# Optimization experiments

Hardware: AMD Instinct MI355X
Metric: run time of the kernel (lower is better)

The kernel has to match this reference:

```python
import jax, jax.numpy as jnp
import numpy as np

M, N, B, L = 512, 2048, 4, 20
H_DENSITY = 0.02  # Tanner graph sparsity: row weight ~N*p=40, col weight ~M*p=10


def setup_inputs() -> dict:
    key = jax.random.key(0)
    ks = jax.random.split(key, 10)
    H = jax.random.bernoulli(ks[0], H_DENSITY, (M, N)).astype(jnp.float32)
    llrs = jax.random.uniform(ks[1], (N,), jnp.float32)
    syndromes = jax.random.randint(ks[2], (B, M, 1), 0, 2, jnp.int32)
    errors = jax.random.randint(ks[3], (B, N), 0, 2, jnp.int32)
    weights_de = jax.random.uniform(ks[4], (L, M, N), jnp.float32)
    weights_llr = jax.random.uniform(ks[5], (L, N), jnp.float32)
    marg_weights_de = jax.random.uniform(ks[6], (L, M, N), jnp.float32)
    marg_weights_llr = jax.random.uniform(ks[7], (L, N), jnp.float32)
    rhos = jnp.ones((L,), jnp.float32)
    residual_weights = jnp.zeros((L,), jnp.float32)
    return dict(syndromes=syndromes, errors=errors, H=H, llrs=llrs,
                weights_de=weights_de, weights_llr=weights_llr,
                marg_weights_de=marg_weights_de, marg_weights_llr=marg_weights_llr,
                rhos=rhos, residual_weights=residual_weights)


def reference(syndromes, errors, H, llrs, weights_de, weights_llr,
              marg_weights_de, marg_weights_llr, rhos, residual_weights):
    batch = syndromes.shape[0]
    m, n = H.shape
    rhos_norm = jax.nn.softmax(rhos)                       # (L,)
    sign = 1.0 - 2.0 * syndromes.astype(H.dtype)           # (B,m,1): (-1)**syndrome
    err_f = errors.astype(H.dtype)                         # (B,n)
    eps = 1e-6

    def step(msgs_dn, xs):
        w_de, w_llr, mw_de, mw_llr, rho, rw = xs
        # error-node (variable) update: column-sum minus self, masked by H
        msgs_en = (H * (llrs * w_llr)
                   + jnp.sum(msgs_dn * w_de, axis=1, keepdims=True)) * H - msgs_dn
        # detector-node (check) update: tanh-product rule with self-exclusion
        d = jnp.tanh(msgs_en * 0.5)
        d = jnp.where(d == 0, jnp.asarray(1.0, d.dtype), d)
        d = jnp.clip(d, -1.0 + eps, 1.0 - eps)
        row_prod = jnp.prod(d, axis=2, keepdims=True)      # (B,m,1)
        msgs_new = 2.0 * jnp.arctanh(row_prod / d) * (sign * H) + rw * msgs_dn
        # marginal beliefs and weighted BCE loss
        beliefs = jnp.sum(msgs_new * mw_de, axis=1) + llrs * mw_llr   # (B,n)
        loss_b = jnp.sum(jax.nn.softplus(beliefs) - (1.0 - err_f) * beliefs, axis=1)
        return msgs_new, rho * loss_b

    init = jnp.zeros((batch, m, n), H.dtype)
    _, losses = jax.lax.scan(
        step, init,
        (weights_de, weights_llr, marg_weights_de, marg_weights_llr,
         rhos_norm, residual_weights))
    return jnp.sum(losses) / batch
```

## Files before the change

kernel.cpp:

```cpp
#include <hip/hip_runtime.h>

#define MM 512
#define NN 2048
#define BB 4
#define LL 20
#define MAXDEG 128
#define NT    1024
#define RR    8
#define COLSB 256
#define SLOTS 4096
#define EPSV  1e-6f

#define WS_ROW_DEG   0
#define WS_ROW_PAD   2048
#define WS_ROW_OFFF  264192
#define WS_DEG_RB    266240
#define WS_RPTR_RB   282624
#define WS_EDGE_CS   299040
#define WS_WDE_P     430112
#define WS_MWDE_P    3051552
#define WS_PP        5672992
#define WS_BAR       5804064

__global__ __launch_bounds__(64)
void build_rows(const float* __restrict__ H, int* __restrict__ row_deg,
                int* __restrict__ row_pad, float* __restrict__ row_offf) {
    int i = blockIdx.x, lane = threadIdx.x;
    const float* hrow = H + (size_t)i * NN;
    float v[32];
    #pragma unroll
    for (int c = 0; c < 32; ++c) v[c] = hrow[c * 64 + lane];
    int base = 0;
    #pragma unroll
    for (int c = 0; c < 32; ++c) {
        bool pred = v[c] != 0.0f;
        unsigned long long mask = __ballot(pred);
        int before = __popcll(mask & ((1ull << lane) - 1ull));
        if (pred) {
            int k = base + before;
            if (k < MAXDEG) row_pad[i * MAXDEG + k] = c * 64 + lane;
        }
        base += __popcll(mask);
    }
    if (lane == 0) {
        row_deg[i] = base < MAXDEG ? base : MAXDEG;
        row_offf[i] = powf(1.0f - EPSV, (float)(NN - base));
    }
}

__global__ __launch_bounds__(512)
void count_slices(const int* __restrict__ row_deg, const int* __restrict__ row_pad,
                  int* __restrict__ deg_rb) {
    int i = threadIdx.x;
    int deg = row_deg[i];
    int cnt[RR];
    #pragma unroll
    for (int r = 0; r < RR; ++r) cnt[r] = 0;
    for (int k = 0; k < deg; ++k) {
        int c = row_pad[i * MAXDEG + k];
        cnt[c >> 8]++;
    }
    #pragma unroll
    for (int r = 0; r < RR; ++r) deg_rb[r * MM + i] = cnt[r];
}

__global__ __launch_bounds__(512)
void scan_slices(const int* __restrict__ deg_rb, int* __restrict__ rptr_rb) {
    __shared__ int tmp[512];
    int r = blockIdx.x, t = threadIdx.x;
    tmp[t] = deg_rb[r * MM + t];
    __syncthreads();
    for (int off = 1; off < 512; off <<= 1) {
        int v = (t >= off) ? tmp[t - off] : 0;
        __syncthreads();
        tmp[t] += v;
        __syncthreads();
    }
    if (t == 0) rptr_rb[r * 513] = 0;
    rptr_rb[r * 513 + t + 1] = tmp[t];
}

__global__ __launch_bounds__(512)
void fill_cs(const int* __restrict__ row_deg, const int* __restrict__ row_pad,
             const int* __restrict__ rptr_rb, unsigned* __restrict__ edge_cs) {
    int i = threadIdx.x;
    int deg = row_deg[i];
    int cnt[RR];
    #pragma unroll
    for (int r = 0; r < RR; ++r) cnt[r] = 0;
    for (int k = 0; k < deg; ++k) {
        int c = row_pad[i * MAXDEG + k];
        int r = c >> 8;
        int pos = rptr_rb[r * 513 + i] + cnt[r]++;
        if (pos < SLOTS)
            edge_cs[r * SLOTS + pos] = ((unsigned)i << 16) | (unsigned)c;
    }
}

__global__ __launch_bounds__(256)
void gather_weights(const float* __restrict__ w_de, const float* __restrict__ mw_de,
                    const unsigned* __restrict__ edge_cs, const int* __restrict__ rptr_rb,
                    float* __restrict__ wde_p, float* __restrict__ mwde_p) {
    int idx = blockIdx.x * 256 + threadIdx.x;
    int l = idx / (RR * SLOTS);
    int rem = idx - l * (RR * SLOTS);
    int r = rem / SLOTS, s = rem - r * SLOTS;
    int tot = rptr_rb[r * 513 + MM];
    if (tot > SLOTS) tot = SLOTS;
    if (s < tot) {
        unsigned pk = edge_cs[r * SLOTS + s];
        size_t src = (size_t)l * MM * NN + (size_t)(pk >> 16) * NN + (pk & 0xffffu);
        wde_p[idx]  = w_de[src];
        mwde_p[idx] = mw_de[src];
    } else {
        wde_p[idx]  = 0.0f;
        mwde_p[idx] = 0.0f;
    }
}

__device__ __forceinline__ void grid_barrier(int* ctr) {
    __syncthreads();
    if (threadIdx.x == 0) {
        asm volatile("s_waitcnt vmcnt(0)" ::: "memory");
        __hip_atomic_fetch_add(ctr, 1, __ATOMIC_RELAXED, __HIP_MEMORY_SCOPE_AGENT);
        int it = 0;
        while (__hip_atomic_load(ctr, __ATOMIC_RELAXED, __HIP_MEMORY_SCOPE_AGENT) < RR) {
            __builtin_amdgcn_s_sleep(1);
            if (++it > (1 << 22)) break;
        }
        asm volatile("" ::: "memory");
    }
    __syncthreads();
}

__global__ __launch_bounds__(NT, 4)
void nbp_main(const int* __restrict__ synd, const int* __restrict__ errs,
              const float* __restrict__ llrs,
              const float* __restrict__ w_llr, const float* __restrict__ mw_llr,
              const float* __restrict__ rhos, const float* __restrict__ resw,
              const int* __restrict__ rptr_rb, const float* __restrict__ row_offf,
              const unsigned* __restrict__ edge_cs,
              const float* __restrict__ wde_p, const float* __restrict__ mwde_p,
              float* __restrict__ pp, int* __restrict__ bar,
              float* __restrict__ out) {
    __shared__ float d_sb[SLOTS];
    __shared__ float colsum_s[COLSB];
    __shared__ float bel_s[COLSB];
    __shared__ float ncs_s[COLSB];
    __shared__ float llrs_s[COLSB];
    __shared__ float ef_s[COLSB];
    __shared__ float rowprod_s[MM];
    __shared__ float rp_coef[MM];
    __shared__ int   rowptr_s[MM + 1];
    __shared__ float rho_n[LL];
    __shared__ float red[16];

    const int blk = blockIdx.x;
    const int b = blk & 3, r = blk >> 2;
    const int tid = threadIdx.x;
    const int lane = tid & 63, wave = tid >> 6;

    int* bar_b = bar + b * 64;

    if (tid == 0) {
        float mx = -1e30f;
        for (int l = 0; l < LL; ++l) mx = fmaxf(mx, rhos[l]);
        float s = 0.0f;
        for (int l = 0; l < LL; ++l) { float e = __expf(rhos[l] - mx); rho_n[l] = e; s += e; }
        for (int l = 0; l < LL; ++l) rho_n[l] /= s;
    }
    if (tid < MM) {
        rowptr_s[tid] = rptr_rb[r * 513 + tid];
        rp_coef[tid] = row_offf[tid] * (1.0f - 2.0f * (float)synd[b * MM + tid]);
    }
    if (tid == MM) rowptr_s[MM] = rptr_rb[r * 513 + MM];
    if (tid < COLSB) {
        int j = r * COLSB + tid;
        float lj = llrs[j];
        llrs_s[tid] = lj;
        colsum_s[tid] = lj * w_llr[j];
        ef_s[tid] = 1.0f - (float)errs[b * NN + j];
        bel_s[tid] = 0.0f;
        ncs_s[tid] = 0.0f;
    }

    int cnt = rptr_rb[r * 513 + MM];
    if (cnt > SLOTS) cnt = SLOTS;
    const int s0 = 4 * tid;

    unsigned idx[4];
    float msg[4], d_r[4];
    #pragma unroll
    for (int k = 0; k < 4; ++k) {
        int e = r * SLOTS + s0 + k;
        idx[k] = edge_cs[(s0 + k) < cnt ? e : r * SLOTS];
        msg[k] = 0.0f;
    }
    __syncthreads();

    float loss = 0.0f;

    for (int l = 0; l < LL; ++l) {
        const float rw = resw[l];
        const int par = l & 1;
        float* pp_b = pp + ((size_t)par * BB + b) * RR * MM;

        const float4 mq = *(const float4*)(mwde_p + ((size_t)(l * RR + r) * SLOTS) + s0);
        float4 wq = make_float4(0.f, 0.f, 0.f, 0.f);
        if (l + 1 < LL)
            wq = *(const float4*)(wde_p + ((size_t)((l + 1) * RR + r) * SLOTS) + s0);
        const float mv[4] = {mq.x, mq.y, mq.z, mq.w};
        const float wn[4] = {wq.x, wq.y, wq.z, wq.w};

        #pragma unroll
        for (int k = 0; k < 4; ++k) {
            int jl = idx[k] & 255u;
            float en = colsum_s[jl] - msg[k];
            float t = __expf(en);
            float d = 1.0f - 2.0f * __builtin_amdgcn_rcpf(t + 1.0f);
            if (d == 0.0f) d = 1.0f;
            d = fminf(fmaxf(d, -1.0f + EPSV), 1.0f - EPSV);
            d_r[k] = d;
        }
        *(float4*)&d_sb[s0] = make_float4(d_r[0], d_r[1], d_r[2], d_r[3]);
        __syncthreads();

        if (tid < MM) {
            int lo = rowptr_s[tid], hi = rowptr_s[tid + 1];
            if (hi > SLOTS) hi = SLOTS;
            float p = 1.0f;
            for (int s = lo; s < hi; ++s) p *= d_sb[s];
            __hip_atomic_store(&pp_b[r * MM + tid], p,
                               __ATOMIC_RELAXED, __HIP_MEMORY_SCOPE_AGENT);
        }
        grid_barrier(&bar_b[l]);

        if (tid < MM) {
            float p = rp_coef[tid];
            #pragma unroll
            for (int r2 = 0; r2 < RR; ++r2)
                p *= __hip_atomic_load(&pp_b[r2 * MM + tid],
                                       __ATOMIC_RELAXED, __HIP_MEMORY_SCOPE_AGENT);
            rowprod_s[tid] = p;
        }
        __syncthreads();

        #pragma unroll
        for (int k = 0; k < 4; ++k) {
            int il = idx[k] >> 16;
            int jl = idx[k] & 255u;
            float rq = rowprod_s[il] * __builtin_amdgcn_rcpf(d_r[k]);
            float v = __logf(1.0f + rq) - __logf(1.0f - rq) + rw * msg[k];
            msg[k] = v;
            if (s0 + k < cnt) {
                atomicAdd(&bel_s[jl], v * mv[k]);
                if (l + 1 < LL) atomicAdd(&ncs_s[jl], v * wn[k]);
            }
        }
        __syncthreads();

        if (tid < COLSB) {
            int j = r * COLSB + tid;
            float bel = llrs_s[tid] * mw_llr[l * NN + j] + bel_s[tid];
            bel_s[tid] = 0.0f;
            float sp = fmaxf(bel, 0.0f) + log1pf(__expf(-fabsf(bel)));
            loss += rho_n[l] * (sp - ef_s[tid] * bel);
            if (l + 1 < LL) {
                colsum_s[tid] = llrs_s[tid] * w_llr[(l + 1) * NN + j] + ncs_s[tid];
                ncs_s[tid] = 0.0f;
            }
        }
        __syncthreads();
    }

    #pragma unroll
    for (int off = 32; off > 0; off >>= 1) loss += __shfl_down(loss, off);
    if (lane == 0) red[wave] = loss;
    __syncthreads();
    if (wave == 0) {
        float v = (lane < 16) ? red[lane] : 0.0f;
        #pragma unroll
        for (int off = 8; off > 0; off >>= 1) v += __shfl_down(v, off);
        if (lane == 0) atomicAdd(out, v * 0.25f);
    }
}

extern "C" void kernel_launch(void* const* d_in, const int* in_sizes, int n_in,
                              void* d_out, int out_size, void* d_ws, size_t ws_size,
                              hipStream_t stream) {
    const int*   synd  = (const int*)  d_in[0];
    const int*   errs  = (const int*)  d_in[1];
    const float* H     = (const float*)d_in[2];
    const float* llrs  = (const float*)d_in[3];
    const float* w_de  = (const float*)d_in[4];
    const float* w_llr = (const float*)d_in[5];
    const float* mw_de = (const float*)d_in[6];
    const float* mw_llr= (const float*)d_in[7];
    const float* rhos  = (const float*)d_in[8];
    const float* resw  = (const float*)d_in[9];

    char* ws = (char*)d_ws;
    int*      row_deg  = (int*)     (ws + WS_ROW_DEG);
    int*      row_pad  = (int*)     (ws + WS_ROW_PAD);
    float*    row_offf = (float*)   (ws + WS_ROW_OFFF);
    int*      deg_rb   = (int*)     (ws + WS_DEG_RB);
    int*      rptr_rb  = (int*)     (ws + WS_RPTR_RB);
    unsigned* edge_cs  = (unsigned*)(ws + WS_EDGE_CS);
    float*    wde_p    = (float*)   (ws + WS_WDE_P);
    float*    mwde_p   = (float*)   (ws + WS_MWDE_P);
    float*    pp       = (float*)   (ws + WS_PP);
    int*      bar      = (int*)     (ws + WS_BAR);
    float*    out      = (float*)d_out;

    hipMemsetAsync(bar, 0, BB * 64 * sizeof(int), stream);
    hipMemsetAsync(d_out, 0, sizeof(float), stream);

    build_rows<<<MM, 64, 0, stream>>>(H, row_deg, row_pad, row_offf);
    count_slices<<<1, 512, 0, stream>>>(row_deg, row_pad, deg_rb);
    scan_slices<<<RR, 512, 0, stream>>>(deg_rb, rptr_rb);
    fill_cs<<<1, 512, 0, stream>>>(row_deg, row_pad, rptr_rb, edge_cs);
    gather_weights<<<(LL * RR * SLOTS) / 256, 256, 0, stream>>>(w_de, mw_de, edge_cs,
                                                                rptr_rb, wde_p, mwde_p);
    nbp_main<<<BB * RR, NT, 0, stream>>>(synd, errs, llrs, w_llr, mw_llr, rhos, resw,
                                         rptr_rb, row_offf, edge_cs, wde_p, mwde_p,
                                         pp, bar, out);
}
```

Before: 454.8 us.

## Fuse graph-build, slicing and weight-gather preprocessing into persistent main kernel

The five preprocessing kernels (row build, slice count, scan, CSR fill, weight gather) are folded into the front of the single persistent 32-block kernel, separated by software grid barriers. This removes five kernel launches and their inter-kernel gaps. In exchange the preprocessing now runs on only 32 blocks instead of many small ones, so the gather and row-build phases have much less parallelism, and it relies on all blocks being co-resident for the spin barriers.

```diff
diff --git a/kernel.cpp b/kernel.cpp
--- a/kernel.cpp
+++ b/kernel.cpp
@@ -6,6 +6,7 @@
 #define LL 20
 #define MAXDEG 128
 #define NT    1024
+#define NBLK  32
 #define RR    8
 #define COLSB 256
 #define SLOTS 4096
@@ -14,108 +15,26 @@
 #define WS_ROW_DEG   0
 #define WS_ROW_PAD   2048
 #define WS_ROW_OFFF  264192
-#define WS_DEG_RB    266240
-#define WS_RPTR_RB   282624
-#define WS_EDGE_CS   299040
-#define WS_WDE_P     430112
-#define WS_MWDE_P    3051552
-#define WS_PP        5672992
-#define WS_BAR       5804064
-
-__global__ __launch_bounds__(64)
-void build_rows(const float* __restrict__ H, int* __restrict__ row_deg,
-                int* __restrict__ row_pad, float* __restrict__ row_offf) {
-    int i = blockIdx.x, lane = threadIdx.x;
-    const float* hrow = H + (size_t)i * NN;
-    float v[32];
-    #pragma unroll
-    for (int c = 0; c < 32; ++c) v[c] = hrow[c * 64 + lane];
-    int base = 0;
-    #pragma unroll
-    for (int c = 0; c < 32; ++c) {
-        bool pred = v[c] != 0.0f;
-        unsigned long long mask = __ballot(pred);
-        int before = __popcll(mask & ((1ull << lane) - 1ull));
-        if (pred) {
-            int k = base + before;
-            if (k < MAXDEG) row_pad[i * MAXDEG + k] = c * 64 + lane;
-        }
-        base += __popcll(mask);
-    }
-    if (lane == 0) {
-        row_deg[i] = base < MAXDEG ? base : MAXDEG;
-        row_offf[i] = powf(1.0f - EPSV, (float)(NN - base));
-    }
-}
-
-__global__ __launch_bounds__(512)
-void count_slices(const int* __restrict__ row_deg, const int* __restrict__ row_pad,
-                  int* __restrict__ deg_rb) {
-    int i = threadIdx.x;
-    int deg = row_deg[i];
-    int cnt[RR];
-    #pragma unroll
-    for (int r = 0; r < RR; ++r) cnt[r] = 0;
-    for (int k = 0; k < deg; ++k) {
-        int c = row_pad[i * MAXDEG + k];
-        cnt[c >> 8]++;
-    }
-    #pragma unroll
-    for (int r = 0; r < RR; ++r) deg_rb[r * MM + i] = cnt[r];
-}
-
-__global__ __launch_bounds__(512)
-void scan_slices(const int* __restrict__ deg_rb, int* __restrict__ rptr_rb) {
-    __shared__ int tmp[512];
-    int r = blockIdx.x, t = threadIdx.x;
-    tmp[t] = deg_rb[r * MM + t];
-    __syncthreads();
-    for (int off = 1; off < 512; off <<= 1) {
-        int v = (t >= off) ? tmp[t - off] : 0;
-        __syncthreads();
-        tmp[t] += v;
-        __syncthreads();
-    }
-    if (t == 0) rptr_rb[r * 513] = 0;
-    rptr_rb[r * 513 + t + 1] = tmp[t];
-}
-
-__global__ __launch_bounds__(512)
-void fill_cs(const int* __restrict__ row_deg, const int* __restrict__ row_pad,
-             const int* __restrict__ rptr_rb, unsigned* __restrict__ edge_cs) {
-    int i = threadIdx.x;
-    int deg = row_deg[i];
-    int cnt[RR];
-    #pragma unroll
-    for (int r = 0; r < RR; ++r) cnt[r] = 0;
-    for (int k = 0; k < deg; ++k) {
-        int c = row_pad[i * MAXDEG + k];
-        int r = c >> 8;
-        int pos = rptr_rb[r * 513 + i] + cnt[r]++;
-        if (pos < SLOTS)
-            edge_cs[r * SLOTS + pos] = ((unsigned)i << 16) | (unsigned)c;
-    }
-}
-
-__global__ __launch_bounds__(256)
-void gather_weights(const float* __restrict__ w_de, const float* __restrict__ mw_de,
-                    const unsigned* __restrict__ edge_cs, const int* __restrict__ rptr_rb,
-                    float* __restrict__ wde_p, float* __restrict__ mwde_p) {
-    int idx = blockIdx.x * 256 + threadIdx.x;
-    int l = idx / (RR * SLOTS);
-    int rem = idx - l * (RR * SLOTS);
-    int r = rem / SLOTS, s = rem - r * SLOTS;
-    int tot = rptr_rb[r * 513 + MM];
-    if (tot > SLOTS) tot = SLOTS;
-    if (s < tot) {
-        unsigned pk = edge_cs[r * SLOTS + s];
-        size_t src = (size_t)l * MM * NN + (size_t)(pk >> 16) * NN + (pk & 0xffffu);
-        wde_p[idx]  = w_de[src];
-        mwde_p[idx] = mw_de[src];
-    } else {
-        wde_p[idx]  = 0.0f;
-        mwde_p[idx] = 0.0f;
-    }
+#define WS_RPTR_RB   266240
+#define WS_EDGE_CS   282880
+#define WS_WDE_P     413952
+#define WS_MWDE_P    3035392
+#define WS_PP        5656832
+#define WS_BAR       5787904
+
+__device__ __forceinline__ void pre_barrier(int* ctr) {
+    __syncthreads();
+    if (threadIdx.x == 0) {
+        __threadfence();
+        __hip_atomic_fetch_add(ctr, 1, __ATOMIC_RELAXED, __HIP_MEMORY_SCOPE_AGENT);
+        int it = 0;
+        while (__hip_atomic_load(ctr, __ATOMIC_RELAXED, __HIP_MEMORY_SCOPE_AGENT) < NBLK) {
+            __builtin_amdgcn_s_sleep(1);
+            if (++it > (1 << 22)) break;
+        }
+        __threadfence();
+    }
+    __syncthreads();
 }
 
 __device__ __forceinline__ void grid_barrier(int* ctr) {
@@ -134,16 +53,19 @@
 }
 
 __global__ __launch_bounds__(NT, 4)
-void nbp_main(const int* __restrict__ synd, const int* __restrict__ errs,
-              const float* __restrict__ llrs,
-              const float* __restrict__ w_llr, const float* __restrict__ mw_llr,
-              const float* __restrict__ rhos, const float* __restrict__ resw,
-              const int* __restrict__ rptr_rb, const float* __restrict__ row_offf,
-              const unsigned* __restrict__ edge_cs,
-              const float* __restrict__ wde_p, const float* __restrict__ mwde_p,
-              float* __restrict__ pp, int* __restrict__ bar,
-              float* __restrict__ out) {
+void nbp_all(const int* __restrict__ synd, const int* __restrict__ errs,
+             const float* __restrict__ H, const float* __restrict__ llrs,
+             const float* __restrict__ w_de, const float* __restrict__ w_llr,
+             const float* __restrict__ mw_de, const float* __restrict__ mw_llr,
+             const float* __restrict__ rhos, const float* __restrict__ resw,
+             int* __restrict__ row_deg, int* __restrict__ row_pad,
+             float* __restrict__ row_offf, int* __restrict__ rptr_rb,
+             unsigned* __restrict__ edge_cs,
+             float* __restrict__ wde_p, float* __restrict__ mwde_p,
+             float* __restrict__ pp, int* __restrict__ bar,
+             float* __restrict__ out) {
     __shared__ float d_sb[SLOTS];
+    __shared__ int   tmp_s[MM];
     __shared__ float colsum_s[COLSB];
     __shared__ float bel_s[COLSB];
     __shared__ float ncs_s[COLSB];
@@ -159,8 +81,87 @@
     const int b = blk & 3, r = blk >> 2;
     const int tid = threadIdx.x;
     const int lane = tid & 63, wave = tid >> 6;
-
     int* bar_b = bar + b * 64;
+    int* pbar  = bar + BB * 64;
+
+    {
+        int i = blk * 16 + wave;
+        const float* hrow = H + (size_t)i * NN;
+        int base = 0;
+        for (int pass = 0; pass < 4; ++pass) {
+            float v[8];
+            #pragma unroll
+            for (int c = 0; c < 8; ++c) v[c] = hrow[(pass * 8 + c) * 64 + lane];
+            #pragma unroll
+            for (int c = 0; c < 8; ++c) {
+                bool pred = v[c] != 0.0f;
+                unsigned long long mask = __ballot(pred);
+                int before = __popcll(mask & ((1ull << lane) - 1ull));
+                if (pred) {
+                    int k = base + before;
+                    if (k < MAXDEG) row_pad[i * MAXDEG + k] = (pass * 8 + c) * 64 + lane;
+                }
+                base += __popcll(mask);
+            }
+        }
+        if (lane == 0) {
+            row_deg[i] = base < MAXDEG ? base : MAXDEG;
+            row_offf[i] = powf(1.0f - EPSV, (float)(NN - base));
+        }
+    }
+    pre_barrier(&pbar[0]);
+
+    if (blk < RR) {
+        const int slice = blk;
+        if (tid < MM) {
+            int deg = row_deg[tid], cnt = 0;
+            for (int k = 0; k < deg; ++k)
+                cnt += ((row_pad[tid * MAXDEG + k] >> 8) == slice);
+            tmp_s[tid] = cnt;
+        }
+        __syncthreads();
+        for (int off = 1; off < MM; off <<= 1) {
+            int v = (tid < MM && tid >= off) ? tmp_s[tid - off] : 0;
+            __syncthreads();
+            if (tid < MM) tmp_s[tid] += v;
+            __syncthreads();
+        }
+        if (tid == 0) rptr_rb[slice * 513] = 0;
+        if (tid < MM) rptr_rb[slice * 513 + tid + 1] = tmp_s[tid];
+        __syncthreads();
+        if (tid < MM) {
+            int deg = row_deg[tid];
+            int pos = (tid == 0) ? 0 : tmp_s[tid - 1];
+            for (int k = 0; k < deg; ++k) {
+                int c = row_pad[tid * MAXDEG + k];
+                if ((c >> 8) == slice && pos < SLOTS) {
+                    edge_cs[slice * SLOTS + pos] = ((unsigned)tid << 16) | (unsigned)c;
+                    ++pos;
+                }
+            }
+        }
+    }
+    pre_barrier(&pbar[1]);
+
+    {
+        int tot = rptr_rb[r * 513 + MM];
+        if (tot > SLOTS) tot = SLOTS;
+        for (int l = b * 5; l < b * 5 + 5; ++l) {
+            for (int s = tid; s < SLOTS; s += NT) {
+                size_t di = ((size_t)(l * RR + r)) * SLOTS + s;
+                if (s < tot) {
+                    unsigned pk = edge_cs[r * SLOTS + s];
+                    size_t src = (size_t)l * MM * NN + (size_t)(pk >> 16) * NN + (pk & 0xffffu);
+                    wde_p[di]  = w_de[src];
+                    mwde_p[di] = mw_de[src];
+                } else {
+                    wde_p[di]  = 0.0f;
+                    mwde_p[di] = 0.0f;
+                }
+            }
+        }
+    }
+    pre_barrier(&pbar[2]);
 
     if (tid == 0) {
         float mx = -1e30f;
@@ -303,7 +304,6 @@
     int*      row_deg  = (int*)     (ws + WS_ROW_DEG);
     int*      row_pad  = (int*)     (ws + WS_ROW_PAD);
     float*    row_offf = (float*)   (ws + WS_ROW_OFFF);
-    int*      deg_rb   = (int*)     (ws + WS_DEG_RB);
     int*      rptr_rb  = (int*)     (ws + WS_RPTR_RB);
     unsigned* edge_cs  = (unsigned*)(ws + WS_EDGE_CS);
     float*    wde_p    = (float*)   (ws + WS_WDE_P);
@@ -312,16 +312,10 @@
     int*      bar      = (int*)     (ws + WS_BAR);
     float*    out      = (float*)d_out;
 
-    hipMemsetAsync(bar, 0, BB * 64 * sizeof(int), stream);
+    hipMemsetAsync(bar, 0, (BB * 64 + 64) * sizeof(int), stream);
     hipMemsetAsync(d_out, 0, sizeof(float), stream);
 
-    build_rows<<<MM, 64, 0, stream>>>(H, row_deg, row_pad, row_offf);
-    count_slices<<<1, 512, 0, stream>>>(row_deg, row_pad, deg_rb);
-    scan_slices<<<RR, 512, 0, stream>>>(deg_rb, rptr_rb);
-    fill_cs<<<1, 512, 0, stream>>>(row_deg, row_pad, rptr_rb, edge_cs);
-    gather_weights<<<(LL * RR * SLOTS) / 256, 256, 0, stream>>>(w_de, mw_de, edge_cs,
-                                                                rptr_rb, wde_p, mwde_p);
-    nbp_main<<<BB * RR, NT, 0, stream>>>(synd, errs, llrs, w_llr, mw_llr, rhos, resw,
-                                         rptr_rb, row_offf, edge_cs, wde_p, mwde_p,
-                                         pp, bar, out);
+    nbp_all<<<NBLK, NT, 0, stream>>>(synd, errs, H, llrs, w_de, w_llr, mw_de, mw_llr,
+                                     rhos, resw, row_deg, row_pad, row_offf, rptr_rb,
+                                     edge_cs, wde_p, mwde_p, pp, bar, out);
 }
```

Result: slower. 470.4 us (+3.4%).
